# Optimization experiments

Measured on AMD Instinct MI355X. Metric: run time of the kernel, lower is better.

## Reference

```python
import jax, jax.numpy as jnp
import numpy as np


def setup_inputs() -> dict:
    key = jax.random.key(0)
    k_x, k_f1, k_f2, k_b = jax.random.split(key, 4)
    N, D = 2097152, 64  # batch rows, in_features = out_features = 8*8
    x = jax.random.normal(k_x, (N, D), dtype=jnp.float32)
    factor1 = jax.random.normal(k_f1, (8, 8), dtype=jnp.float32)
    factor2 = jax.random.normal(k_f2, (8, 8), dtype=jnp.float32)
    bias = jax.random.normal(k_b, (D,), dtype=jnp.float32)
    return {"x": x, "factor1": factor1, "factor2": factor2, "bias": bias}


def reference(x, factor1, factor2, bias):
    # weight = kron(ones((1,1)), factor1, factor2) == kron(factor1, factor2)
    # shape: [8*8, 8*8] = [64, 64]
    w = jnp.kron(factor1, factor2)
    # F.linear(x, w, bias) = x @ w.T + bias
    return x @ w.T + bias
```

## Files before the change

### kernel.cpp

```cpp
#include <hip/hip_runtime.h>


#define GLD_TO_LDS16(gptr, lptr)                                          \
    __builtin_amdgcn_global_load_lds(                                     \
        (const __attribute__((address_space(1))) unsigned int*)(gptr),    \
        (__attribute__((address_space(3))) unsigned int*)(lptr), 16, 0, 0)

__global__ __launch_bounds__(256, 4) void kron_linear_kernel(
    const float* __restrict__ x,
    const float* __restrict__ f1,
    const float* __restrict__ f2,
    const float* __restrict__ bias,
    float* __restrict__ out,
    int n_rows)
{
    const int t = threadIdx.x;
    const long long tile_row0 = (long long)blockIdx.x * 128;

    __shared__ float4 lds[2048];

    if (tile_row0 + 128 <= (long long)n_rows) {
        const int r = t & 127;
        const int h = t >> 7;

        const float4* xg = (const float4*)x + tile_row0 * 16;
#pragma unroll
        for (int k = 0; k < 8; ++k) {
            int s  = k * 256 + t;
            int sr = s >> 4;
            int c  = (s & 15) ^ (sr & 15);
            GLD_TO_LDS16(xg + (sr * 16 + c), &lds[s]);
        }
        __syncthreads();

        const float* f2h = f2 + (h * 4) * 8;
        float T[8][4];
        const int rbase = r * 16;
        const int rs = r & 15;
#pragma unroll
        for (int i1 = 0; i1 < 8; ++i1) {
            float4 a = lds[rbase + ((2 * i1)     ^ rs)];
            float4 b = lds[rbase + ((2 * i1 + 1) ^ rs)];
            float xv[8] = {a.x, a.y, a.z, a.w, b.x, b.y, b.z, b.w};
#pragma unroll
            for (int jj = 0; jj < 4; ++jj) {
                float acc = 0.f;
#pragma unroll
                for (int i2 = 0; i2 < 8; ++i2)
                    acc += xv[i2] * f2h[jj * 8 + i2];
                T[i1][jj] = acc;
            }
        }
        __syncthreads();

#pragma unroll
        for (int j1 = 0; j1 < 8; ++j1) {
            float o0 = bias[j1 * 8 + 4 * h + 0];
            float o1 = bias[j1 * 8 + 4 * h + 1];
            float o2 = bias[j1 * 8 + 4 * h + 2];
            float o3 = bias[j1 * 8 + 4 * h + 3];
#pragma unroll
            for (int i1 = 0; i1 < 8; ++i1) {
                float w = f1[j1 * 8 + i1];
                o0 += w * T[i1][0];
                o1 += w * T[i1][1];
                o2 += w * T[i1][2];
                o3 += w * T[i1][3];
            }
            int c = 2 * j1 + h;
            lds[rbase + (c ^ rs)] = make_float4(o0, o1, o2, o3);
        }
        __syncthreads();

        float4* og = (float4*)out + tile_row0 * 16;
#pragma unroll
        for (int k = 0; k < 8; ++k) {
            int s  = k * 256 + t;
            int sr = s >> 4;
            int c  = (s & 15) ^ (sr & 15);
            og[sr * 16 + c] = lds[s];
        }
    } else {
        long long row = tile_row0 + t;
        if (row >= (long long)n_rows) return;

        const float* xr = x + (size_t)row * 64;
        float* orow = out + (size_t)row * 64;

        float T[8][8];
#pragma unroll
        for (int i1 = 0; i1 < 8; ++i1) {
            float4 a = *(const float4*)(xr + i1 * 8);
            float4 b = *(const float4*)(xr + i1 * 8 + 4);
            float xv[8] = {a.x, a.y, a.z, a.w, b.x, b.y, b.z, b.w};
#pragma unroll
            for (int j2 = 0; j2 < 8; ++j2) {
                float acc = 0.f;
#pragma unroll
                for (int i2 = 0; i2 < 8; ++i2)
                    acc += xv[i2] * f2[j2 * 8 + i2];
                T[i1][j2] = acc;
            }
        }
#pragma unroll
        for (int j1 = 0; j1 < 8; ++j1) {
            float o[8];
#pragma unroll
            for (int j2 = 0; j2 < 8; ++j2) o[j2] = bias[j1 * 8 + j2];
#pragma unroll
            for (int i1 = 0; i1 < 8; ++i1) {
                float w = f1[j1 * 8 + i1];
#pragma unroll
                for (int j2 = 0; j2 < 8; ++j2)
                    o[j2] += w * T[i1][j2];
            }
            *(float4*)(orow + j1 * 8)     = make_float4(o[0], o[1], o[2], o[3]);
            *(float4*)(orow + j1 * 8 + 4) = make_float4(o[4], o[5], o[6], o[7]);
        }
    }
}

extern "C" void kernel_launch(void* const* d_in, const int* in_sizes, int n_in,
                              void* d_out, int out_size, void* d_ws, size_t ws_size,
                              hipStream_t stream) {
    const float* x    = (const float*)d_in[0];
    const float* f1   = (const float*)d_in[1];
    const float* f2   = (const float*)d_in[2];
    const float* bias = (const float*)d_in[3];
    float* out = (float*)d_out;

    int n_rows = out_size / 64;
    int blocks = (n_rows + 127) / 128;
    kron_linear_kernel<<<blocks, 256, 0, stream>>>(x, f1, f2, bias, out, n_rows);
}
```

Baseline: 855.2 us.

## Halve tile to 64 rows, four threads per row, drop sync, nontemporal stores

Each block now handles 64 rows instead of 128. Each row is split across four lanes of the same wavefront, and every lane computes two output columns per group. This lets the launch bounds ask for 8 blocks per CU and lowers the per-thread register count (T0/T1 instead of T[8][4]). Because a row's readers and writers are all in one wave, the barrier between reading x from LDS and writing results back is replaced with a compiler memory fence. Output stores use nontemporal hints to reduce cache pollution. The trade-offs are more blocks in the grid, and correctness now depends on LDS operations within a wave staying in order.

```diff
diff --git a/kernel.cpp b/kernel.cpp
--- a/kernel.cpp
+++ b/kernel.cpp
@@ -1,12 +1,14 @@
 #include <hip/hip_runtime.h>
 
+
+typedef float vfloat4 __attribute__((ext_vector_type(4)));
 
 #define GLD_TO_LDS16(gptr, lptr)                                          \
     __builtin_amdgcn_global_load_lds(                                     \
         (const __attribute__((address_space(1))) unsigned int*)(gptr),    \
         (__attribute__((address_space(3))) unsigned int*)(lptr), 16, 0, 0)
 
-__global__ __launch_bounds__(256, 4) void kron_linear_kernel(
+__global__ __launch_bounds__(256, 8) void kron_linear_kernel(
     const float* __restrict__ x,
     const float* __restrict__ f1,
     const float* __restrict__ f2,
@@ -15,17 +17,17 @@
     int n_rows)
 {
     const int t = threadIdx.x;
-    const long long tile_row0 = (long long)blockIdx.x * 128;
+    const long long tile_row0 = (long long)blockIdx.x * 64;
 
-    __shared__ float4 lds[2048];
+    __shared__ vfloat4 lds[1024];
 
-    if (tile_row0 + 128 <= (long long)n_rows) {
-        const int r = t & 127;
-        const int h = t >> 7;
+    if (tile_row0 + 64 <= (long long)n_rows) {
+        const int r = t >> 2;
+        const int q = t & 3;
 
-        const float4* xg = (const float4*)x + tile_row0 * 16;
+        const vfloat4* xg = (const vfloat4*)x + tile_row0 * 16;
 #pragma unroll
-        for (int k = 0; k < 8; ++k) {
+        for (int k = 0; k < 4; ++k) {
             int s  = k * 256 + t;
             int sr = s >> 4;
             int c  = (s & 15) ^ (sr & 15);
@@ -33,52 +35,51 @@
         }
         __syncthreads();
 
-        const float* f2h = f2 + (h * 4) * 8;
-        float T[8][4];
+        const float* f2a = f2 + (2 * q) * 8;
+        const float* f2b = f2 + (2 * q + 1) * 8;
+        float T0[8], T1[8];
         const int rbase = r * 16;
         const int rs = r & 15;
 #pragma unroll
         for (int i1 = 0; i1 < 8; ++i1) {
-            float4 a = lds[rbase + ((2 * i1)     ^ rs)];
-            float4 b = lds[rbase + ((2 * i1 + 1) ^ rs)];
+            vfloat4 a = lds[rbase + ((2 * i1)     ^ rs)];
+            vfloat4 b = lds[rbase + ((2 * i1 + 1) ^ rs)];
             float xv[8] = {a.x, a.y, a.z, a.w, b.x, b.y, b.z, b.w};
+            float acc0 = 0.f, acc1 = 0.f;
 #pragma unroll
-            for (int jj = 0; jj < 4; ++jj) {
-                float acc = 0.f;
+            for (int i2 = 0; i2 < 8; ++i2) {
+                acc0 += xv[i2] * f2a[i2];
+                acc1 += xv[i2] * f2b[i2];
+            }
+            T0[i1] = acc0;
+            T1[i1] = acc1;
+        }
+
+        asm volatile("" ::: "memory");
+
+        float2* lds2 = (float2*)lds;
 #pragma unroll
-                for (int i2 = 0; i2 < 8; ++i2)
-                    acc += xv[i2] * f2h[jj * 8 + i2];
-                T[i1][jj] = acc;
+        for (int j1 = 0; j1 < 8; ++j1) {
+            float o0 = bias[j1 * 8 + 2 * q];
+            float o1 = bias[j1 * 8 + 2 * q + 1];
+#pragma unroll
+            for (int i1 = 0; i1 < 8; ++i1) {
+                float w = f1[j1 * 8 + i1];
+                o0 += w * T0[i1];
+                o1 += w * T1[i1];
             }
+            int c = 2 * j1 + (q >> 1);
+            lds2[(rbase + (c ^ rs)) * 2 + (q & 1)] = make_float2(o0, o1);
         }
         __syncthreads();
 
+        vfloat4* og = (vfloat4*)out + tile_row0 * 16;
 #pragma unroll
-        for (int j1 = 0; j1 < 8; ++j1) {
-            float o0 = bias[j1 * 8 + 4 * h + 0];
-            float o1 = bias[j1 * 8 + 4 * h + 1];
-            float o2 = bias[j1 * 8 + 4 * h + 2];
-            float o3 = bias[j1 * 8 + 4 * h + 3];
-#pragma unroll
-            for (int i1 = 0; i1 < 8; ++i1) {
-                float w = f1[j1 * 8 + i1];
-                o0 += w * T[i1][0];
-                o1 += w * T[i1][1];
-                o2 += w * T[i1][2];
-                o3 += w * T[i1][3];
-            }
-            int c = 2 * j1 + h;
-            lds[rbase + (c ^ rs)] = make_float4(o0, o1, o2, o3);
-        }
-        __syncthreads();
-
-        float4* og = (float4*)out + tile_row0 * 16;
-#pragma unroll
-        for (int k = 0; k < 8; ++k) {
+        for (int k = 0; k < 4; ++k) {
             int s  = k * 256 + t;
             int sr = s >> 4;
             int c  = (s & 15) ^ (sr & 15);
-            og[sr * 16 + c] = lds[s];
+            __builtin_nontemporal_store(lds[s], og + (sr * 16 + c));
         }
     } else {
         long long row = tile_row0 + t;
@@ -130,6 +131,6 @@
     float* out = (float*)d_out;
 
     int n_rows = out_size / 64;
-    int blocks = (n_rows + 127) / 128;
+    int blocks = (n_rows + 63) / 64;
     kron_linear_kernel<<<blocks, 256, 0, stream>>>(x, f1, f2, bias, out, n_rows);
 }
```

New measurement: 844.3 us. No clear change (-1.3%).
